# Performance work log

Measured on AMD Instinct MI355X. Metric: run time of the kernel, lower is better.

The kernel has to match this reference:

```python
import jax, jax.numpy as jnp
import numpy as np

N, G, E, F, H = 65536, 32768, 600000, 128, 128

def _mlp(x, w1, b1, w2, b2):
    # Linear -> SiLU -> Linear
    return jax.nn.silu(x @ w1 + b1) @ w2 + b2

def setup_inputs() -> dict:
    key = jax.random.key(0)
    ks = jax.random.split(key, 24)
    def lin(k, din, dout):
        kw, kb = jax.random.split(k)
        s = 1.0 / np.sqrt(din)
        return (jax.random.uniform(kw, (din, dout), jnp.float32, -s, s),
                jax.random.uniform(kb, (dout,), jnp.float32, -s, s))
    nm_w1, nm_b1 = lin(ks[0], F, H)
    nm_w2, nm_b2 = lin(ks[1], H, H)
    em_w1, em_b1 = lin(ks[2], 6, H)
    em_w2, em_b2 = lin(ks[3], H, H)
    mm_w1, mm_b1 = lin(ks[4], 2 * H, H)
    mm_w2, mm_b2 = lin(ks[5], H, H)
    um_w1, um_b1 = lin(ks[6], H, H)
    um_w2, um_b2 = lin(ks[7], H, H)
    return {
        "node_features": jax.random.normal(ks[8], (N, F), jnp.float32),
        "node_pos": jax.random.uniform(ks[9], (N, 3), jnp.float32),
        "grid_pos": jax.random.uniform(ks[10], (G, 3), jnp.float32),
        "edge_index": jax.random.randint(ks[11], (2, E), 0, G, jnp.int64),
        "nm_w1": nm_w1, "nm_b1": nm_b1, "nm_w2": nm_w2, "nm_b2": nm_b2,
        "em_w1": em_w1, "em_b1": em_b1, "em_w2": em_w2, "em_b2": em_b2,
        "mm_w1": mm_w1, "mm_b1": mm_b1, "mm_w2": mm_w2, "mm_b2": mm_b2,
        "um_w1": um_w1, "um_b1": um_b1, "um_w2": um_w2, "um_b2": um_b2,
    }

def reference(node_features, node_pos, grid_pos, edge_index,
              nm_w1, nm_b1, nm_w2, nm_b2,
              em_w1, em_b1, em_w2, em_b2,
              mm_w1, mm_b1, mm_w2, mm_b2,
              um_w1, um_b1, um_w2, um_b2):
    src, tgt = edge_index[0], edge_index[1]
    # node_model on all points [N,H]
    nf = _mlp(node_features, nm_w1, nm_b1, nm_w2, nm_b2)
    # edge features from gathered positions [E,6] -> [E,H]
    edge_attr = jnp.concatenate([node_pos[src], grid_pos[tgt]], axis=-1)
    ef = _mlp(edge_attr, em_w1, em_b1, em_w2, em_b2)
    # messages [E,2H] -> [E,H]
    msg = _mlp(jnp.concatenate([nf[src], ef], axis=-1), mm_w1, mm_b1, mm_w2, mm_b2)
    # scatter-add mean aggregation to grid [G,H]
    counts = jax.ops.segment_sum(jnp.ones((msg.shape[0],), msg.dtype), tgt, num_segments=G)
    counts = jnp.maximum(counts, 1.0)[:, None]
    agg = jax.ops.segment_sum(msg, tgt, num_segments=G) / counts
    # update_model [G,H]
    return _mlp(agg, um_w1, um_b1, um_w2, um_b2)
```

## Files before the change

### kernel.cpp

```cpp
#include <hip/hip_runtime.h>

#define N_NODES 65536
#define G_GRID  32768
#define E_EDGES 600000
#define HD      128

typedef __attribute__((ext_vector_type(8))) short bf8;
typedef __attribute__((ext_vector_type(4))) float f32x4;

__device__ __forceinline__ short f2bf(float f){
  union { float f; unsigned u; } v; v.f = f;
  unsigned r = v.u + 0x7FFFu + ((v.u >> 16) & 1u);
  return (short)(r >> 16);
}
__device__ __forceinline__ float bf2f(short s){
  union { unsigned u; float f; } v; v.u = ((unsigned)(unsigned short)s) << 16; return v.f;
}

__device__ __forceinline__ bf8 load_pack8(const float* p, float scale){
  float4 u0 = *(const float4*)p;
  float4 u1 = *(const float4*)(p + 4);
  bf8 r;
  r[0]=f2bf(u0.x*scale); r[1]=f2bf(u0.y*scale); r[2]=f2bf(u0.z*scale); r[3]=f2bf(u0.w*scale);
  r[4]=f2bf(u1.x*scale); r[5]=f2bf(u1.y*scale); r[6]=f2bf(u1.z*scale); r[7]=f2bf(u1.w*scale);
  return r;
}

__global__ void setup_k(const float* __restrict__ nmw1, const float* __restrict__ nmw2,
                        const float* __restrict__ mmw1, const float* __restrict__ mmw2,
                        const float* __restrict__ umw1, const float* __restrict__ umw2,
                        const float* __restrict__ emw1, const float* __restrict__ eb1,
                        const float* __restrict__ emw2, const float* __restrict__ eb2,
                        const float* __restrict__ mb1,
                        const int* __restrict__ eidx,
                        short* __restrict__ wts, short* __restrict__ wcombot,
                        float* __restrict__ bcombo, short* __restrict__ ew1x,
                        int* __restrict__ counts)
{
  const int b = blockIdx.x;
  if (b < 512){
    int i = b*256 + threadIdx.x;
    const float* src; int local; bool k256 = false;
    if      (i < 16384){ src = nmw1; local = i; }
    else if (i < 32768){ src = nmw2; local = i - 16384; }
    else if (i < 49152){ src = emw2; local = i - 32768; }
    else if (i < 81920){ src = mmw1; local = i - 49152; k256 = true; }
    else if (i < 98304){ src = mmw2; local = i - 81920; }
    else if (i < 114688){ src = umw1; local = i - 98304; }
    else               { src = umw2; local = i - 114688; }
    int n, k;
    if (k256){ n = local >> 8; k = local & 255; }
    else     { n = local >> 7; k = local & 127; }
    wts[i] = f2bf(src[k*HD + n]);
  } else if (b < 640){
    __shared__ float part[2][128];
    int k = b - 512;
    int t = threadIdx.x, n = t & 127, half = t >> 7;
    float acc = 0.f;
    const float* er = emw2 + k*HD + half*64;
    #pragma unroll 8
    for (int j=0;j<64;j++) acc += er[j] * mmw1[(HD + half*64 + j)*HD + n];
    part[half][n] = acc;
    __syncthreads();
    if (half == 0) wcombot[n*HD + k] = f2bf(part[0][n] + part[1][n]);
  } else if (b == 640){
    int t = threadIdx.x;
    if (t < 128){
      int n = t;
      float acc = mb1[n];
      for (int j=0;j<HD;j++) acc += eb2[j] * mmw1[(HD + j)*HD + n];
      bcombo[n] = acc;
      short v[32];
      #pragma unroll
      for (int i=0;i<32;i++) v[i] = 0;
      #pragma unroll
      for (int i=0;i<6;i++){
        float wv = emw1[i*HD + n];
        short wh = f2bf(wv);
        short wl = f2bf(wv - bf2f(wh));
        v[i] = wh; v[6+i] = wh; v[12+i] = wl;
      }
      float bv = eb1[n];
      short bh = f2bf(bv);
      v[18] = bh; v[19] = f2bf(bv - bf2f(bh));
      #pragma unroll
      for (int i=0;i<32;i++) ew1x[n*32 + i] = v[i];
    }
  } else {
    int e = (b - 641)*256 + threadIdx.x;
    if (e < E_EDGES) atomicAdd(&counts[eidx[E_EDGES + e]], 1);
  }
}

__global__ void node_mlp_k(const float* __restrict__ X,
                           const short* __restrict__ w1t, const float* __restrict__ b1,
                           const short* __restrict__ w2t, const float* __restrict__ b2,
                           short* __restrict__ nf)
{
  __shared__ short hid[64][136];
  const int t = threadIdx.x;
  const int wave = t >> 6, lane = t & 63, l15 = lane & 15, q = lane >> 4;
  const int rw = blockIdx.x*64 + wave*16;

  bf8 a[4];
  const float* xr = X + (size_t)(rw + l15)*HD;
  #pragma unroll
  for (int kt=0; kt<4; kt++) a[kt] = load_pack8(xr + kt*32 + q*8, 1.0f);

  #pragma unroll
  for (int ct=0; ct<8; ct++){
    f32x4 acc = {0.f,0.f,0.f,0.f};
    #pragma unroll
    for (int kt=0; kt<4; kt++){
      bf8 b = *(const bf8*)(w1t + (ct*16 + l15)*HD + kt*32 + q*8);
      acc = __builtin_amdgcn_mfma_f32_16x16x32_bf16(a[kt], b, acc, 0, 0, 0);
    }
    float bias = b1[ct*16 + l15];
    #pragma unroll
    for (int r=0;r<4;r++){
      float v = acc[r] + bias;
      v = v / (1.f + __expf(-v));
      hid[wave*16 + q*4 + r][ct*16 + l15] = f2bf(v);
    }
  }
  bf8 a2[4];
  #pragma unroll
  for (int kt=0;kt<4;kt++) a2[kt] = *(const bf8*)&hid[wave*16 + l15][kt*32 + q*8];
  #pragma unroll
  for (int ct=0; ct<8; ct++){
    f32x4 acc = {0.f,0.f,0.f,0.f};
    #pragma unroll
    for (int kt=0;kt<4;kt++){
      bf8 b = *(const bf8*)(w2t + (ct*16 + l15)*HD + kt*32 + q*8);
      acc = __builtin_amdgcn_mfma_f32_16x16x32_bf16(a2[kt], b, acc, 0, 0, 0);
    }
    float bias = b2[ct*16 + l15];
    #pragma unroll
    for (int r=0;r<4;r++)
      nf[(size_t)(rw + q*4 + r)*HD + ct*16 + l15] = f2bf(acc[r] + bias);
  }
}

__global__ void scan_k(const int* __restrict__ counts, int* __restrict__ offs){
  __shared__ int part[1024];
  const int t = threadIdx.x;
  const int base = t*32;
  int loc[32];
  int s = 0;
  #pragma unroll
  for (int i=0;i<32;i++){ loc[i] = s; s += counts[base+i]; }
  part[t] = s;
  __syncthreads();
  for (int off=1; off<1024; off<<=1){
    int v = (t>=off) ? part[t-off] : 0;
    __syncthreads();
    part[t] += v;
    __syncthreads();
  }
  int pre = (t==0) ? 0 : part[t-1];
  #pragma unroll
  for (int i=0;i<32;i++) offs[base+i] = pre + loc[i];
  if (t==1023) offs[G_GRID] = pre + s;
}

__global__ void scatter_k(const int* __restrict__ eidx, const int* __restrict__ offs,
                          int* __restrict__ counts,
                          int* __restrict__ srcs_s, int* __restrict__ tgts_s,
                          const float* __restrict__ npos, const float* __restrict__ gpos,
                          float* __restrict__ pos6){
  int e = blockIdx.x*256 + threadIdx.x;
  if (e < E_EDGES){
    int s = eidx[e];
    int g = eidx[E_EDGES + e];
    int slot = offs[g] + atomicSub(&counts[g], 1) - 1;
    srcs_s[slot] = s;
    tgts_s[slot] = g;
    float* pd = pos6 + (size_t)slot*8;
    pd[0]=npos[s*3+0]; pd[1]=npos[s*3+1]; pd[2]=npos[s*3+2];
    pd[3]=gpos[g*3+0]; pd[4]=gpos[g*3+1]; pd[5]=gpos[g*3+2];
    pd[6]=0.f; pd[7]=0.f;
  }
}

__device__ __forceinline__ bf8 build_af(const float p[6], int q){
  short ph[6], pl[6];
  #pragma unroll
  for (int i=0;i<6;i++){
    ph[i] = f2bf(p[i]);
    pl[i] = f2bf(p[i] - bf2f(ph[i]));
  }
  bf8 af = {0,0,0,0,0,0,0,0};
  if (q == 0){
    af[0]=ph[0]; af[1]=ph[1]; af[2]=ph[2]; af[3]=ph[3];
    af[4]=ph[4]; af[5]=ph[5]; af[6]=pl[0]; af[7]=pl[1];
  } else if (q == 1){
    af[0]=pl[2]; af[1]=pl[3]; af[2]=pl[4]; af[3]=pl[5];
    af[4]=ph[0]; af[5]=ph[1]; af[6]=ph[2]; af[7]=ph[3];
  } else if (q == 2){
    af[0]=ph[4]; af[1]=ph[5]; af[2]=(short)0x3F80; af[3]=(short)0x3F80;
  }
  return af;
}

__device__ __forceinline__ void seg_flush(const f32x4& acc, unsigned m, int tr,
                                          int q, int col, bool owner,
                                          float* __restrict__ agg)
{
  if (m == 0u){
    float s = (acc[0] + acc[1]) + (acc[2] + acc[3]);
    s += __shfl_xor(s, 16);
    s += __shfl_xor(s, 32);
    int tg = __shfl(tr, 0);
    if (owner) atomicAdd(&agg[(size_t)tg*HD + col], s);
  } else {
    unsigned mm = m;
    int lo = 0;
    while (true){
      int hi = mm ? (int)__builtin_ctz(mm) : 16;
      float s = 0.f;
      #pragma unroll
      for (int r=0;r<4;r++){
        int row = q*4 + r;
        s += (row >= lo && row < hi) ? acc[r] : 0.f;
      }
      s += __shfl_xor(s, 16);
      s += __shfl_xor(s, 32);
      int tg = __shfl(tr, lo);
      if (owner) atomicAdd(&agg[(size_t)tg*HD + col], s);
      if (!mm) break;
      lo = hi; mm &= mm - 1;
    }
  }
}

__global__ void __launch_bounds__(256, 4)
edge_msg8_k(const int* __restrict__ srcs_s, const int* __restrict__ tgts_s,
            const float* __restrict__ pos6,
            const short* __restrict__ ew1x, const float* __restrict__ bcombo,
            const short* __restrict__ mw1t, const short* __restrict__ wcombot,
            const short* __restrict__ mw2t,
            const short* __restrict__ nf, float* __restrict__ agg)
{
  __shared__ short hm[64][136];

  const int t = threadIdx.x;
  const int w = t >> 6, lane = t & 63, l15 = lane & 15, q = lane >> 4;
  const int base = blockIdx.x*128 + w*32;
  if (base >= E_EDGES) return;
  const int w16 = w*16;

  const int i0 = base + l15, i1 = base + 16 + l15;
  const int s0 = srcs_s[i0], s1 = srcs_s[i1];
  const int tr0 = tgts_s[i0], tr1 = tgts_s[i1];

  bf8 an0[4], an1[4];
  {
    const short* n0p = nf + (size_t)s0*HD + q*8;
    const short* n1p = nf + (size_t)s1*HD + q*8;
    #pragma unroll
    for (int kt=0;kt<4;kt++){ an0[kt] = *(const bf8*)(n0p + kt*32); an1[kt] = *(const bf8*)(n1p + kt*32); }
  }
  float pA[6], pB[6];
  {
    const float* pp = pos6 + (size_t)i0*8;
    f32x4 u0 = *(const f32x4*)pp;
    f32x4 u1 = *(const f32x4*)(pp + 4);
    pA[0]=u0[0]; pA[1]=u0[1]; pA[2]=u0[2]; pA[3]=u0[3]; pA[4]=u1[0]; pA[5]=u1[1];
    const float* pq = pos6 + (size_t)i1*8;
    f32x4 v0 = *(const f32x4*)pq;
    f32x4 v1 = *(const f32x4*)(pq + 4);
    pB[0]=v0[0]; pB[1]=v0[1]; pB[2]=v0[2]; pB[3]=v0[3]; pB[4]=v1[0]; pB[5]=v1[1];
  }

  int p0 = __shfl_up(tr0, 1);
  int p1 = __shfl_up(tr1, 1);
  unsigned m0 = (unsigned)__ballot(l15 > 0 && tr0 != p0) & 0xFFFFu;
  unsigned m1 = (unsigned)__ballot(l15 > 0 && tr1 != p1) & 0xFFFFu;

  bf8 af0 = build_af(pA, q);
  bf8 af1 = build_af(pB, q);
  bf8 ah0[4], ah1[4];
  #pragma unroll
  for (int ct=0; ct<8; ct++){
    bf8 bw = *(const bf8*)(ew1x + (ct*16 + l15)*32 + q*8);
    f32x4 h = {0.f,0.f,0.f,0.f};
    h = __builtin_amdgcn_mfma_f32_16x16x32_bf16(af0, bw, h, 0,0,0);
    const int col = ct*16 + l15;
    #pragma unroll
    for (int r=0;r<4;r++){
      float v = h[r];
      v = v / (1.f + __expf(-v));
      hm[w16 + q*4 + r][col] = f2bf(v);
    }
  }
  #pragma unroll
  for (int kt=0;kt<4;kt++) ah0[kt] = *(const bf8*)&hm[w16 + l15][kt*32 + q*8];
  #pragma unroll
  for (int ct=0; ct<8; ct++){
    bf8 bw = *(const bf8*)(ew1x + (ct*16 + l15)*32 + q*8);
    f32x4 h = {0.f,0.f,0.f,0.f};
    h = __builtin_amdgcn_mfma_f32_16x16x32_bf16(af1, bw, h, 0,0,0);
    const int col = ct*16 + l15;
    #pragma unroll
    for (int r=0;r<4;r++){
      float v = h[r];
      v = v / (1.f + __expf(-v));
      hm[w16 + q*4 + r][col] = f2bf(v);
    }
  }
  #pragma unroll
  for (int kt=0;kt<4;kt++) ah1[kt] = *(const bf8*)&hm[w16 + l15][kt*32 + q*8];

  unsigned t1p[16];
  #pragma unroll
  for (int ct=0; ct<8; ct++){
    bf8 bw1[4], bwc[4];
    #pragma unroll
    for (int kt=0;kt<4;kt++){
      bw1[kt] = *(const bf8*)(mw1t + (ct*16 + l15)*256 + kt*32 + q*8);
      bwc[kt] = *(const bf8*)(wcombot + (ct*16 + l15)*HD + kt*32 + q*8);
    }
    f32x4 acc0 = {0.f,0.f,0.f,0.f}, acc1 = {0.f,0.f,0.f,0.f};
    #pragma unroll
    for (int kt=0;kt<4;kt++){
      acc0 = __builtin_amdgcn_mfma_f32_16x16x32_bf16(an0[kt], bw1[kt], acc0, 0,0,0);
      acc1 = __builtin_amdgcn_mfma_f32_16x16x32_bf16(an1[kt], bw1[kt], acc1, 0,0,0);
    }
    #pragma unroll
    for (int kt=0;kt<4;kt++){
      acc0 = __builtin_amdgcn_mfma_f32_16x16x32_bf16(ah0[kt], bwc[kt], acc0, 0,0,0);
      acc1 = __builtin_amdgcn_mfma_f32_16x16x32_bf16(ah1[kt], bwc[kt], acc1, 0,0,0);
    }
    float bias = bcombo[ct*16 + l15];
    const int col = ct*16 + l15;
    #pragma unroll
    for (int r=0;r<4;r++){
      float v = acc0[r] + bias;
      v = v / (1.f + __expf(-v));
      hm[w16 + q*4 + r][col] = f2bf(v);
    }
    #pragma unroll
    for (int rr=0; rr<2; rr++){
      float va = acc1[2*rr]     + bias;
      float vb = acc1[2*rr + 1] + bias;
      va = va / (1.f + __expf(-va));
      vb = vb / (1.f + __expf(-vb));
      t1p[ct*2 + rr] = (unsigned)(unsigned short)f2bf(va)
                     | ((unsigned)(unsigned short)f2bf(vb) << 16);
    }
  }
  bf8 am0[4], am1[4];
  #pragma unroll
  for (int kt=0;kt<4;kt++) am0[kt] = *(const bf8*)&hm[w16 + l15][kt*32 + q*8];
  #pragma unroll
  for (int ct=0; ct<8; ct++){
    const int col = ct*16 + l15;
    #pragma unroll
    for (int rr=0; rr<2; rr++){
      unsigned p = t1p[ct*2 + rr];
      hm[w16 + q*4 + 2*rr    ][col] = (short)(p & 0xFFFFu);
      hm[w16 + q*4 + 2*rr + 1][col] = (short)(p >> 16);
    }
  }
  #pragma unroll
  for (int kt=0;kt<4;kt++) am1[kt] = *(const bf8*)&hm[w16 + l15][kt*32 + q*8];

  #pragma unroll
  for (int ct=0; ct<8; ct++){
    bf8 bw[4];
    #pragma unroll
    for (int kt=0;kt<4;kt++)
      bw[kt] = *(const bf8*)(mw2t + (ct*16 + l15)*HD + kt*32 + q*8);
    f32x4 acc0 = {0.f,0.f,0.f,0.f}, acc1 = {0.f,0.f,0.f,0.f};
    #pragma unroll
    for (int kt=0;kt<4;kt++){
      acc0 = __builtin_amdgcn_mfma_f32_16x16x32_bf16(am0[kt], bw[kt], acc0, 0,0,0);
      acc1 = __builtin_amdgcn_mfma_f32_16x16x32_bf16(am1[kt], bw[kt], acc1, 0,0,0);
    }
    const int col = ct*16 + l15;
    const bool owner = (q == (ct & 3));
    seg_flush(acc0, m0, tr0, q, col, owner, agg);
    seg_flush(acc1, m1, tr1, q, col, owner, agg);
  }
}

__global__ void update_mlp2_k(const float* __restrict__ agg, const int* __restrict__ offs,
                              const short* __restrict__ w1t, const float* __restrict__ b1,
                              const short* __restrict__ w2t, const float* __restrict__ b2,
                              const float* __restrict__ mb2,
                              float* __restrict__ out)
{
  __shared__ short hid[64][136];
  const int t = threadIdx.x;
  const int wave = t >> 6, lane = t & 63, l15 = lane & 15, q = lane >> 4;
  const int rw = blockIdx.x*64 + wave*16;

  int row = rw + l15;
  int cnt = offs[row+1] - offs[row];
  float rcp = 1.0f / fmaxf((float)cnt, 1.0f);
  float bsc = (cnt > 0) ? 1.0f : 0.0f;
  bf8 a[4];
  const float* ar = agg + (size_t)row*HD;
  #pragma unroll
  for (int kt=0; kt<4; kt++){
    const float* p  = ar  + kt*32 + q*8;
    const float* mp = mb2 + kt*32 + q*8;
    float4 u0 = *(const float4*)p;   float4 u1 = *(const float4*)(p + 4);
    float4 m0v = *(const float4*)mp; float4 m1v = *(const float4*)(mp + 4);
    bf8 r;
    r[0]=f2bf(u0.x*rcp + m0v.x*bsc); r[1]=f2bf(u0.y*rcp + m0v.y*bsc);
    r[2]=f2bf(u0.z*rcp + m0v.z*bsc); r[3]=f2bf(u0.w*rcp + m0v.w*bsc);
    r[4]=f2bf(u1.x*rcp + m1v.x*bsc); r[5]=f2bf(u1.y*rcp + m1v.y*bsc);
    r[6]=f2bf(u1.z*rcp + m1v.z*bsc); r[7]=f2bf(u1.w*rcp + m1v.w*bsc);
    a[kt] = r;
  }

  #pragma unroll
  for (int ct=0; ct<8; ct++){
    f32x4 acc = {0.f,0.f,0.f,0.f};
    #pragma unroll
    for (int kt=0; kt<4; kt++){
      bf8 b = *(const bf8*)(w1t + (ct*16 + l15)*HD + kt*32 + q*8);
      acc = __builtin_amdgcn_mfma_f32_16x16x32_bf16(a[kt], b, acc, 0, 0, 0);
    }
    float bias = b1[ct*16 + l15];
    #pragma unroll
    for (int r=0;r<4;r++){
      float v = acc[r] + bias;
      v = v / (1.f + __expf(-v));
      hid[wave*16 + q*4 + r][ct*16 + l15] = f2bf(v);
    }
  }
  bf8 a2[4];
  #pragma unroll
  for (int kt=0;kt<4;kt++) a2[kt] = *(const bf8*)&hid[wave*16 + l15][kt*32 + q*8];
  #pragma unroll
  for (int ct=0; ct<8; ct++){
    f32x4 acc = {0.f,0.f,0.f,0.f};
    #pragma unroll
    for (int kt=0;kt<4;kt++){
      bf8 b = *(const bf8*)(w2t + (ct*16 + l15)*HD + kt*32 + q*8);
      acc = __builtin_amdgcn_mfma_f32_16x16x32_bf16(a2[kt], b, acc, 0, 0, 0);
    }
    float bias = b2[ct*16 + l15];
    #pragma unroll
    for (int r=0;r<4;r++)
      out[(size_t)(rw + q*4 + r)*HD + ct*16 + l15] = acc[r] + bias;
  }
}

extern "C" void kernel_launch(void* const* d_in, const int* in_sizes, int n_in,
                              void* d_out, int out_size, void* d_ws, size_t ws_size,
                              hipStream_t stream)
{
  const float* node_features = (const float*)d_in[0];
  const float* node_pos      = (const float*)d_in[1];
  const float* grid_pos      = (const float*)d_in[2];
  const int*   edge_index    = (const int*)d_in[3];
  const float* nm_w1 = (const float*)d_in[4];
  const float* nm_b1 = (const float*)d_in[5];
  const float* nm_w2 = (const float*)d_in[6];
  const float* nm_b2 = (const float*)d_in[7];
  const float* em_w1 = (const float*)d_in[8];
  const float* em_b1 = (const float*)d_in[9];
  const float* em_w2 = (const float*)d_in[10];
  const float* em_b2 = (const float*)d_in[11];
  const float* mm_w1 = (const float*)d_in[12];
  const float* mm_b1 = (const float*)d_in[13];
  const float* mm_w2 = (const float*)d_in[14];
  const float* mm_b2 = (const float*)d_in[15];
  const float* um_w1 = (const float*)d_in[16];
  const float* um_b1 = (const float*)d_in[17];
  const float* um_w2 = (const float*)d_in[18];
  const float* um_b2 = (const float*)d_in[19];
  float* out = (float*)d_out;

  char* ws = (char*)d_ws;
  short* nf     = (short*)ws;
  int*   counts = (int*)  (ws + 16777216ull);
  int*   offs   = (int*)  (ws + 16908288ull);
  short* wts    = (short*)(ws + 17039424ull);
  short* wcombot= (short*)(ws + 17301568ull);
  float* bcombo = (float*)(ws + 17334336ull);
  short* ew1x   = (short*)(ws + 17334848ull);
  int*   srcs_s = (int*)  (ws + 17343040ull);
  int*   tgts_s = (int*)  (ws + 19743040ull);
  float* pos6   = (float*)(ws + 22143040ull);

  short* nmw1t = wts;
  short* nmw2t = wts + 16384;
  short* mmw1t = wts + 49152;
  short* mmw2t = wts + 81920;
  short* umw1t = wts + 98304;
  short* umw2t = wts + 114688;

  float* agg = out;

  (void)hipMemsetAsync(counts, 0, 131072, stream);
  (void)hipMemsetAsync(out, 0, (size_t)G_GRID*HD*4, stream);

  const int count_blocks = (E_EDGES + 255)/256;
  setup_k<<<641 + count_blocks, 256, 0, stream>>>(nm_w1, nm_w2, mm_w1, mm_w2, um_w1, um_w2,
      em_w1, em_b1, em_w2, em_b2, mm_b1, edge_index, wts, wcombot, bcombo, ew1x, counts);
  node_mlp_k<<<G_GRID/64, 256, 0, stream>>>(node_features, nmw1t, nm_b1, nmw2t, nm_b2, nf);
  scan_k<<<1, 1024, 0, stream>>>(counts, offs);
  scatter_k<<<count_blocks, 256, 0, stream>>>(edge_index, offs, counts, srcs_s, tgts_s,
      node_pos, grid_pos, pos6);
  edge_msg8_k<<<(E_EDGES + 127)/128, 256, 0, stream>>>(srcs_s, tgts_s, pos6,
      ew1x, bcombo, mmw1t, wcombot, mmw2t, nf, agg);
  update_mlp2_k<<<G_GRID/64, 256, 0, stream>>>(agg, offs, umw1t, um_b1, umw2t, um_b2, mm_b2, out);
}
```

Measured before the change: 530.8 us.

## Process edge sub-tiles sequentially to cut registers and raise occupancy

Rewrites the edge message kernel to handle its two 16-edge sub-tiles one after another through shared front/back helpers, instead of interleaving both tiles' MFMA chains. This removes the duplicate live fragment arrays and the packed temporary buffer, so launch bounds can be raised from 4 to 5 waves per SIMD. The second tile's gathers are issued after the first tile's front half so their latency can overlap with compute. In exchange, weight fragments are reloaded once per tile instead of being shared across both tiles, and the per-wave instruction-level parallelism between the two tiles is lost.

```diff
diff --git a/kernel.cpp b/kernel.cpp
--- a/kernel.cpp
+++ b/kernel.cpp
@@ -233,8 +233,76 @@
   }
 }
 
-__global__ void __launch_bounds__(256, 4)
-edge_msg8_k(const int* __restrict__ srcs_s, const int* __restrict__ tgts_s,
+__device__ __forceinline__ void tile_front(int w16, int l15, int q,
+    bf8 af, const bf8* an,
+    const short* __restrict__ ew1x, const float* __restrict__ bcombo,
+    const short* __restrict__ mw1t, const short* __restrict__ wcombot,
+    short (*hm)[136])
+{
+  #pragma unroll
+  for (int ct=0; ct<8; ct++){
+    bf8 bw = *(const bf8*)(ew1x + (ct*16 + l15)*32 + q*8);
+    f32x4 h = {0.f,0.f,0.f,0.f};
+    h = __builtin_amdgcn_mfma_f32_16x16x32_bf16(af, bw, h, 0,0,0);
+    const int col = ct*16 + l15;
+    #pragma unroll
+    for (int r=0;r<4;r++){
+      float v = h[r];
+      v = v / (1.f + __expf(-v));
+      hm[w16 + q*4 + r][col] = f2bf(v);
+    }
+  }
+  bf8 ah[4];
+  #pragma unroll
+  for (int kt=0;kt<4;kt++) ah[kt] = *(const bf8*)&hm[w16 + l15][kt*32 + q*8];
+
+  #pragma unroll
+  for (int ct=0; ct<8; ct++){
+    f32x4 acc = {0.f,0.f,0.f,0.f};
+    #pragma unroll
+    for (int kt=0;kt<4;kt++){
+      bf8 b1v = *(const bf8*)(mw1t + (ct*16 + l15)*256 + kt*32 + q*8);
+      acc = __builtin_amdgcn_mfma_f32_16x16x32_bf16(an[kt], b1v, acc, 0,0,0);
+    }
+    #pragma unroll
+    for (int kt=0;kt<4;kt++){
+      bf8 bcv = *(const bf8*)(wcombot + (ct*16 + l15)*HD + kt*32 + q*8);
+      acc = __builtin_amdgcn_mfma_f32_16x16x32_bf16(ah[kt], bcv, acc, 0,0,0);
+    }
+    float bias = bcombo[ct*16 + l15];
+    const int col = ct*16 + l15;
+    #pragma unroll
+    for (int r=0;r<4;r++){
+      float v = acc[r] + bias;
+      v = v / (1.f + __expf(-v));
+      hm[w16 + q*4 + r][col] = f2bf(v);
+    }
+  }
+}
+
+__device__ __forceinline__ void tile_back(int w16, int l15, int q,
+    unsigned m, int tr,
+    const short* __restrict__ mw2t, short (*hm)[136], float* __restrict__ agg)
+{
+  bf8 am[4];
+  #pragma unroll
+  for (int kt=0;kt<4;kt++) am[kt] = *(const bf8*)&hm[w16 + l15][kt*32 + q*8];
+  #pragma unroll
+  for (int ct=0; ct<8; ct++){
+    f32x4 acc = {0.f,0.f,0.f,0.f};
+    #pragma unroll
+    for (int kt=0;kt<4;kt++){
+      bf8 b = *(const bf8*)(mw2t + (ct*16 + l15)*HD + kt*32 + q*8);
+      acc = __builtin_amdgcn_mfma_f32_16x16x32_bf16(am[kt], b, acc, 0,0,0);
+    }
+    const int col = ct*16 + l15;
+    const bool owner = (q == (ct & 3));
+    seg_flush(acc, m, tr, q, col, owner, agg);
+  }
+}
+
+__global__ void __launch_bounds__(256, 5)
+edge_msg9_k(const int* __restrict__ srcs_s, const int* __restrict__ tgts_s,
             const float* __restrict__ pos6,
             const short* __restrict__ ew1x, const float* __restrict__ bcombo,
             const short* __restrict__ mw1t, const short* __restrict__ wcombot,
@@ -249,139 +317,59 @@
   if (base >= E_EDGES) return;
   const int w16 = w*16;
 
-  const int i0 = base + l15, i1 = base + 16 + l15;
-  const int s0 = srcs_s[i0], s1 = srcs_s[i1];
-  const int tr0 = tgts_s[i0], tr1 = tgts_s[i1];
-
-  bf8 an0[4], an1[4];
+  const int i0 = base + l15;
+  const int s0 = srcs_s[i0];
+  const int tr0 = tgts_s[i0];
+  bf8 an0[4];
   {
     const short* n0p = nf + (size_t)s0*HD + q*8;
-    const short* n1p = nf + (size_t)s1*HD + q*8;
-    #pragma unroll
-    for (int kt=0;kt<4;kt++){ an0[kt] = *(const bf8*)(n0p + kt*32); an1[kt] = *(const bf8*)(n1p + kt*32); }
-  }
-  float pA[6], pB[6];
+    #pragma unroll
+    for (int kt=0;kt<4;kt++) an0[kt] = *(const bf8*)(n0p + kt*32);
+  }
+  bf8 af0;
   {
+    float pA[6];
     const float* pp = pos6 + (size_t)i0*8;
     f32x4 u0 = *(const f32x4*)pp;
     f32x4 u1 = *(const f32x4*)(pp + 4);
     pA[0]=u0[0]; pA[1]=u0[1]; pA[2]=u0[2]; pA[3]=u0[3]; pA[4]=u1[0]; pA[5]=u1[1];
+    af0 = build_af(pA, q);
+  }
+  unsigned m0;
+  {
+    int p = __shfl_up(tr0, 1);
+    m0 = (unsigned)__ballot(l15 > 0 && tr0 != p) & 0xFFFFu;
+  }
+
+  tile_front(w16, l15, q, af0, an0, ew1x, bcombo, mw1t, wcombot, hm);
+
+  const int i1 = base + 16 + l15;
+  const int s1 = srcs_s[i1];
+  const int tr1 = tgts_s[i1];
+  bf8 an1[4];
+  {
+    const short* n1p = nf + (size_t)s1*HD + q*8;
+    #pragma unroll
+    for (int kt=0;kt<4;kt++) an1[kt] = *(const bf8*)(n1p + kt*32);
+  }
+  bf8 af1;
+  {
+    float pB[6];
     const float* pq = pos6 + (size_t)i1*8;
     f32x4 v0 = *(const f32x4*)pq;
     f32x4 v1 = *(const f32x4*)(pq + 4);
     pB[0]=v0[0]; pB[1]=v0[1]; pB[2]=v0[2]; pB[3]=v0[3]; pB[4]=v1[0]; pB[5]=v1[1];
-  }
-
-  int p0 = __shfl_up(tr0, 1);
-  int p1 = __shfl_up(tr1, 1);
-  unsigned m0 = (unsigned)__ballot(l15 > 0 && tr0 != p0) & 0xFFFFu;
-  unsigned m1 = (unsigned)__ballot(l15 > 0 && tr1 != p1) & 0xFFFFu;
-
-  bf8 af0 = build_af(pA, q);
-  bf8 af1 = build_af(pB, q);
-  bf8 ah0[4], ah1[4];
-  #pragma unroll
-  for (int ct=0; ct<8; ct++){
-    bf8 bw = *(const bf8*)(ew1x + (ct*16 + l15)*32 + q*8);
-    f32x4 h = {0.f,0.f,0.f,0.f};
-    h = __builtin_amdgcn_mfma_f32_16x16x32_bf16(af0, bw, h, 0,0,0);
-    const int col = ct*16 + l15;
-    #pragma unroll
-    for (int r=0;r<4;r++){
-      float v = h[r];
-      v = v / (1.f + __expf(-v));
-      hm[w16 + q*4 + r][col] = f2bf(v);
-    }
-  }
-  #pragma unroll
-  for (int kt=0;kt<4;kt++) ah0[kt] = *(const bf8*)&hm[w16 + l15][kt*32 + q*8];
-  #pragma unroll
-  for (int ct=0; ct<8; ct++){
-    bf8 bw = *(const bf8*)(ew1x + (ct*16 + l15)*32 + q*8);
-    f32x4 h = {0.f,0.f,0.f,0.f};
-    h = __builtin_amdgcn_mfma_f32_16x16x32_bf16(af1, bw, h, 0,0,0);
-    const int col = ct*16 + l15;
-    #pragma unroll
-    for (int r=0;r<4;r++){
-      float v = h[r];
-      v = v / (1.f + __expf(-v));
-      hm[w16 + q*4 + r][col] = f2bf(v);
-    }
-  }
-  #pragma unroll
-  for (int kt=0;kt<4;kt++) ah1[kt] = *(const bf8*)&hm[w16 + l15][kt*32 + q*8];
-
-  unsigned t1p[16];
-  #pragma unroll
-  for (int ct=0; ct<8; ct++){
-    bf8 bw1[4], bwc[4];
-    #pragma unroll
-    for (int kt=0;kt<4;kt++){
-      bw1[kt] = *(const bf8*)(mw1t + (ct*16 + l15)*256 + kt*32 + q*8);
-      bwc[kt] = *(const bf8*)(wcombot + (ct*16 + l15)*HD + kt*32 + q*8);
-    }
-    f32x4 acc0 = {0.f,0.f,0.f,0.f}, acc1 = {0.f,0.f,0.f,0.f};
-    #pragma unroll
-    for (int kt=0;kt<4;kt++){
-      acc0 = __builtin_amdgcn_mfma_f32_16x16x32_bf16(an0[kt], bw1[kt], acc0, 0,0,0);
-      acc1 = __builtin_amdgcn_mfma_f32_16x16x32_bf16(an1[kt], bw1[kt], acc1, 0,0,0);
-    }
-    #pragma unroll
-    for (int kt=0;kt<4;kt++){
-      acc0 = __builtin_amdgcn_mfma_f32_16x16x32_bf16(ah0[kt], bwc[kt], acc0, 0,0,0);
-      acc1 = __builtin_amdgcn_mfma_f32_16x16x32_bf16(ah1[kt], bwc[kt], acc1, 0,0,0);
-    }
-    float bias = bcombo[ct*16 + l15];
-    const int col = ct*16 + l15;
-    #pragma unroll
-    for (int r=0;r<4;r++){
-      float v = acc0[r] + bias;
-      v = v / (1.f + __expf(-v));
-      hm[w16 + q*4 + r][col] = f2bf(v);
-    }
-    #pragma unroll
-    for (int rr=0; rr<2; rr++){
-      float va = acc1[2*rr]     + bias;
-      float vb = acc1[2*rr + 1] + bias;
-      va = va / (1.f + __expf(-va));
-      vb = vb / (1.f + __expf(-vb));
-      t1p[ct*2 + rr] = (unsigned)(unsigned short)f2bf(va)
-                     | ((unsigned)(unsigned short)f2bf(vb) << 16);
-    }
-  }
-  bf8 am0[4], am1[4];
-  #pragma unroll
-  for (int kt=0;kt<4;kt++) am0[kt] = *(const bf8*)&hm[w16 + l15][kt*32 + q*8];
-  #pragma unroll
-  for (int ct=0; ct<8; ct++){
-    const int col = ct*16 + l15;
-    #pragma unroll
-    for (int rr=0; rr<2; rr++){
-      unsigned p = t1p[ct*2 + rr];
-      hm[w16 + q*4 + 2*rr    ][col] = (short)(p & 0xFFFFu);
-      hm[w16 + q*4 + 2*rr + 1][col] = (short)(p >> 16);
-    }
-  }
-  #pragma unroll
-  for (int kt=0;kt<4;kt++) am1[kt] = *(const bf8*)&hm[w16 + l15][kt*32 + q*8];
-
-  #pragma unroll
-  for (int ct=0; ct<8; ct++){
-    bf8 bw[4];
-    #pragma unroll
-    for (int kt=0;kt<4;kt++)
-      bw[kt] = *(const bf8*)(mw2t + (ct*16 + l15)*HD + kt*32 + q*8);
-    f32x4 acc0 = {0.f,0.f,0.f,0.f}, acc1 = {0.f,0.f,0.f,0.f};
-    #pragma unroll
-    for (int kt=0;kt<4;kt++){
-      acc0 = __builtin_amdgcn_mfma_f32_16x16x32_bf16(am0[kt], bw[kt], acc0, 0,0,0);
-      acc1 = __builtin_amdgcn_mfma_f32_16x16x32_bf16(am1[kt], bw[kt], acc1, 0,0,0);
-    }
-    const int col = ct*16 + l15;
-    const bool owner = (q == (ct & 3));
-    seg_flush(acc0, m0, tr0, q, col, owner, agg);
-    seg_flush(acc1, m1, tr1, q, col, owner, agg);
-  }
+    af1 = build_af(pB, q);
+  }
+  unsigned m1;
+  {
+    int p = __shfl_up(tr1, 1);
+    m1 = (unsigned)__ballot(l15 > 0 && tr1 != p) & 0xFFFFu;
+  }
+
+  tile_back(w16, l15, q, m0, tr0, mw2t, hm, agg);
+  tile_front(w16, l15, q, af1, an1, ew1x, bcombo, mw1t, wcombot, hm);
+  tile_back(w16, l15, q, m1, tr1, mw2t, hm, agg);
 }
 
 __global__ void update_mlp2_k(const float* __restrict__ agg, const int* __restrict__ offs,
@@ -506,7 +494,7 @@
   scan_k<<<1, 1024, 0, stream>>>(counts, offs);
   scatter_k<<<count_blocks, 256, 0, stream>>>(edge_index, offs, counts, srcs_s, tgts_s,
       node_pos, grid_pos, pos6);
-  edge_msg8_k<<<(E_EDGES + 127)/128, 256, 0, stream>>>(srcs_s, tgts_s, pos6,
+  edge_msg9_k<<<(E_EDGES + 127)/128, 256, 0, stream>>>(srcs_s, tgts_s, pos6,
       ew1x, bcombo, mmw1t, wcombot, mmw2t, nf, agg);
   update_mlp2_k<<<G_GRID/64, 256, 0, stream>>>(agg, offs, umw1t, um_b1, umw2t, um_b2, mm_b2, out);
 }
```

Result: slower. 1.084 ms (+104.1%).
